# Kernel tuning notes

Hardware: AMD Instinct MI355X
Metric: run time of the kernel (lower is better)

Reference implementation:

```python
import jax, jax.numpy as jnp
import numpy as np

N, L, D = 8, 2048, 128


def setup_inputs() -> dict:
    key = jax.random.key(0)
    k1, k2, k3, k4 = jax.random.split(key, 4)
    x_t = jax.random.normal(k1, (N, L, D), jnp.float32)
    x_f = jax.random.normal(k2, (N, L, D), jnp.float32)
    W = jax.random.normal(k3, (D, D), jnp.float32) / np.sqrt(D)  # proj weight (torch Linear layout)
    b = jax.random.normal(k4, (D,), jnp.float32) * 0.02
    return {"x_t": x_t, "x_f": x_f, "W": W, "b": b}


def _col_score(a, c, scale):
    # softmax attention with zeroed diagonal, then column-sum -> [N, L]
    att = jnp.einsum('nld,nmd->nlm', a, c) * scale
    att = jax.nn.softmax(att, axis=-1)
    att = att * (1.0 - jnp.eye(att.shape[-1], dtype=att.dtype))
    return jnp.sum(att, axis=1)


def _mask(score, time):
    # score: [N, L]; k-th extreme threshold, k = L//2
    k = int(0.5 * score.shape[1])
    if time:
        vals, _ = jax.lax.top_k(score, k)          # k largest, descending
        theta = vals[:, -1:]                        # k-th largest
        return score > theta
    else:
        vals, _ = jax.lax.top_k(-score, k)          # k smallest
        theta = -vals[:, -1:]                       # k-th smallest
        return score <= theta


def reference(x_t, x_f, W, b):
    scale = 1.0 / np.sqrt(W.shape[0])
    pt = x_t @ W.T + b
    pf = x_f @ W.T + b
    score_t = _col_score(pt, pt, scale)
    score_f = _col_score(pf, pf, scale)
    score_tf = _col_score(pt, pf, scale)
    score_ft = _col_score(pf, pt, scale)
    mask_t = _mask(score_t, False)
    mask_f = _mask(score_f, False)
    mask_tf = _mask(score_tf, True)   # computed in original forward (unused in blend)
    mask_ft = _mask(score_ft, True)
    mask_t1 = (mask_t & ~mask_f)[:, :, None]   # [N, L, 1] broadcast over D
    mask_f1 = (mask_f & ~mask_t)[:, :, None]
    x_t1 = jnp.where(mask_t1, x_f, x_t)
    x_f1 = jnp.where(mask_f1, x_t, x_f)
    return (0.5 * (x_t1 + x_t), 0.5 * (x_f1 + x_f))
```

## Files before the change

### kernel.cpp

```cpp
#include <hip/hip_runtime.h>
#include <math.h>

#define LL 2048
#define DD 128
#define NS 16
#define SLAB (LL * DD)
#define SCALE 0.08838834764831845f
#define NT 16
#define NPAIR 136

typedef __attribute__((ext_vector_type(8))) short short8v;
typedef __attribute__((ext_vector_type(4))) float float4v;

__device__ __forceinline__ unsigned int f2bf(float f) {
    unsigned int u = __float_as_uint(f);
    u += 0x7fffu + ((u >> 16) & 1u);
    return u >> 16;
}
__device__ __forceinline__ void pair_decode(int p, int& ib, int& jb) {
    int i = 0;
    while (p >= NT - i) { p -= NT - i; ++i; }
    ib = i; jb = i + p;
}

__device__ __forceinline__ void work_decode(int bx, int by, int& pair, int& ns) {
    const int lin = by * NPAIR + bx;
    const int xcd = lin & 7;
    const int wi  = lin >> 3;
    const int h   = (wi >= NPAIR) ? 1 : 0;
    ns   = xcd + 8 * h;
    pair = wi - NPAIR * h;
}

__device__ __forceinline__ void gl_lds16(const void* g, void* l) {
    __builtin_amdgcn_global_load_lds(
        (const __attribute__((address_space(1))) void*)g,
        (__attribute__((address_space(3))) void*)l, 16, 0, 0);
}

__device__ __forceinline__ void stage_panel(
    const unsigned short* __restrict__ gT, unsigned short* lbuf, int tid)
{
#pragma unroll
    for (int it = 0; it < 2; ++it) {
        const int s   = tid + it * 256;
        const int sb  = (tid & ~63) + it * 256;
        const int row = s >> 2;
        const int oc  = (s & 3) ^ ((row >> 1) & 3);
        gl_lds16(gT + (size_t)row * DD + oc * 8, lbuf + (size_t)sb * 8);
    }
}

__global__ __launch_bounds__(256, 4) void proj_kernel(
    const float* __restrict__ xt, const float* __restrict__ xf,
    const float* __restrict__ W,  const float* __restrict__ bias,
    unsigned short* __restrict__ Ph, unsigned short* __restrict__ Pl)
{
    __shared__ float Alds[64 * 36];
    __shared__ float Blds[128 * 36];
    __shared__ float bs[128];
    const int ns = blockIdx.y;
    const int l0 = blockIdx.x * 64;
    const int src = ns >> 3, n = ns & 7;
    const float* x = (src ? xf : xt) + (size_t)n * LL * DD;
    const int tid = threadIdx.x;
    const int ty = tid >> 4, tx = tid & 15;

    if (tid < 128) bs[tid] = bias[tid];
    __syncthreads();

    float acc[4][8];
#pragma unroll
    for (int i = 0; i < 4; ++i)
#pragma unroll
        for (int j = 0; j < 8; ++j) acc[i][j] = bs[tx + 16 * j];

    for (int kc = 0; kc < 4; ++kc) {
        __syncthreads();
#pragma unroll
        for (int t = 0; t < 2; ++t) {
            int idx = tid + t * 256;
            int r = idx >> 3, k4 = (idx & 7) << 2;
            *(float4*)&Alds[r * 36 + k4] =
                *(const float4*)&x[(size_t)(l0 + r) * DD + kc * 32 + k4];
        }
#pragma unroll
        for (int t = 0; t < 4; ++t) {
            int idx = tid + t * 256;
            int r = idx >> 3, k4 = (idx & 7) << 2;
            *(float4*)&Blds[r * 36 + k4] =
                *(const float4*)&W[(size_t)r * DD + kc * 32 + k4];
        }
        __syncthreads();
#pragma unroll
        for (int k4 = 0; k4 < 32; k4 += 4) {
            float4 a4[4], b4[8];
#pragma unroll
            for (int i = 0; i < 4; ++i) a4[i] = *(const float4*)&Alds[(ty + 16 * i) * 36 + k4];
#pragma unroll
            for (int j = 0; j < 8; ++j) b4[j] = *(const float4*)&Blds[(tx + 16 * j) * 36 + k4];
#pragma unroll
            for (int i = 0; i < 4; ++i)
#pragma unroll
                for (int j = 0; j < 8; ++j) {
                    acc[i][j] = fmaf(a4[i].x, b4[j].x, acc[i][j]);
                    acc[i][j] = fmaf(a4[i].y, b4[j].y, acc[i][j]);
                    acc[i][j] = fmaf(a4[i].z, b4[j].z, acc[i][j]);
                    acc[i][j] = fmaf(a4[i].w, b4[j].w, acc[i][j]);
                }
        }
    }
#pragma unroll
    for (int i = 0; i < 4; ++i) {
        const size_t rowo = (size_t)ns * SLAB + (size_t)(l0 + ty + 16 * i) * DD;
#pragma unroll
        for (int j = 0; j < 8; ++j) {
            float p = acc[i][j];
            unsigned int hb = f2bf(p);
            float hf = __uint_as_float(hb << 16);
            unsigned int lb = f2bf(p - hf);
            Ph[rowo + tx + 16 * j] = (unsigned short)hb;
            Pl[rowo + tx + 16 * j] = (unsigned short)lb;
        }
    }
}

__device__ __forceinline__ void mfma_core(
    const unsigned short* __restrict__ Ph, const unsigned short* __restrict__ Pl,
    int ns, int ib, int jb, int tid,
    unsigned short (*pan)[4096],
    float4v (&acc)[4][4])
{
    const int lane = tid & 63;
    const int quad = lane >> 4, l16 = lane & 15;
    const int wave = tid >> 6;
    const int wr = wave >> 1, wc = wave & 1;
    const bool dg = (ib == jb);

    const unsigned short* sAh = Ph + (size_t)ns * SLAB + (size_t)ib * 128 * DD;
    const unsigned short* sAl = Pl + (size_t)ns * SLAB + (size_t)ib * 128 * DD;
    const unsigned short* sBh = Ph + (size_t)ns * SLAB + (size_t)jb * 128 * DD;
    const unsigned short* sBl = Pl + (size_t)ns * SLAB + (size_t)jb * 128 * DD;

    const unsigned short* alp[4];
#pragma unroll
    for (int rt = 0; rt < 4; ++rt)
        alp[rt] = sAl + (size_t)(wr * 64 + rt * 16 + l16) * DD + quad * 8;

#pragma unroll
    for (int i = 0; i < 4; ++i)
#pragma unroll
        for (int j = 0; j < 4; ++j)
#pragma unroll
            for (int r = 0; r < 4; ++r) acc[i][j][r] = 0.f;

    stage_panel(sAh, pan[0], tid);
    if (!dg) stage_panel(sBh, pan[1], tid);
    stage_panel(sBl, pan[2], tid);
    short8v alr[2][4];
#pragma unroll
    for (int rt = 0; rt < 4; ++rt) alr[0][rt] = *(const short8v*)&alp[rt][0];
    __syncthreads();

#pragma unroll
    for (int kc = 0; kc < 4; ++kc) {
        const int cur = (kc & 1) * 3;
        if (kc < 3) {
            const int nxt = ((kc + 1) & 1) * 3;
            stage_panel(sAh + (kc + 1) * 32, pan[nxt + 0], tid);
            if (!dg) stage_panel(sBh + (kc + 1) * 32, pan[nxt + 1], tid);
            stage_panel(sBl + (kc + 1) * 32, pan[nxt + 2], tid);
#pragma unroll
            for (int rt = 0; rt < 4; ++rt)
                alr[(kc + 1) & 1][rt] = *(const short8v*)&alp[rt][(kc + 1) * 32];
        }
        const unsigned short* AhP = pan[cur + 0];
        const unsigned short* BhP = dg ? pan[cur + 0] : pan[cur + 1];
        const unsigned short* BlP = pan[cur + 2];

        short8v ah[4], bh[4], bl[4];
#pragma unroll
        for (int rt = 0; rt < 4; ++rt) {
            const int r = wr * 64 + rt * 16 + l16;
            const int off = r * 32 + ((quad ^ ((r >> 1) & 3)) << 3);
            ah[rt] = *(const short8v*)&AhP[off];
        }
#pragma unroll
        for (int ct = 0; ct < 4; ++ct) {
            const int r = wc * 64 + ct * 16 + l16;
            const int off = r * 32 + ((quad ^ ((r >> 1) & 3)) << 3);
            bh[ct] = *(const short8v*)&BhP[off];
            bl[ct] = *(const short8v*)&BlP[off];
        }
        __builtin_amdgcn_s_setprio(1);
#pragma unroll
        for (int rt = 0; rt < 4; ++rt)
#pragma unroll
            for (int ct = 0; ct < 4; ++ct) {
                acc[rt][ct] = __builtin_amdgcn_mfma_f32_16x16x32_bf16(ah[rt], bh[ct], acc[rt][ct], 0, 0, 0);
                acc[rt][ct] = __builtin_amdgcn_mfma_f32_16x16x32_bf16(ah[rt], bl[ct], acc[rt][ct], 0, 0, 0);
                acc[rt][ct] = __builtin_amdgcn_mfma_f32_16x16x32_bf16(alr[kc & 1][rt], bh[ct], acc[rt][ct], 0, 0, 0);
            }
        __builtin_amdgcn_s_setprio(0);
        if (kc < 3) __syncthreads();
    }
}

__global__ __launch_bounds__(256, 3) void stats_kernel(
    const unsigned short* __restrict__ Ph, const unsigned short* __restrict__ Pl,
    float* __restrict__ Zpart)
{
    __shared__ unsigned short pan[6][4096];
    __shared__ float Zr[128][2], Zc[128][2];
    int pair, ns;  work_decode(blockIdx.x, blockIdx.y, pair, ns);
    int ib, jb;    pair_decode(pair, ib, jb);
    const int tid = threadIdx.x;
    const int lane = tid & 63, quad = lane >> 4, l16 = lane & 15, wave = tid >> 6;
    const int wr = wave >> 1, wc = wave & 1;

    float4v acc[4][4];
    mfma_core(Ph, Pl, ns, ib, jb, tid, pan, acc);

    float cs[4] = {0.f, 0.f, 0.f, 0.f};
#pragma unroll
    for (int rt = 0; rt < 4; ++rt)
#pragma unroll
        for (int rg = 0; rg < 4; ++rg) {
            float e[4];
            float s = 0.f;
#pragma unroll
            for (int ct = 0; ct < 4; ++ct) {
                e[ct] = __expf(acc[rt][ct][rg] * SCALE);
                s += e[ct]; cs[ct] += e[ct];
            }
            s += __shfl_xor(s, 1);
            s += __shfl_xor(s, 2);
            s += __shfl_xor(s, 4);
            s += __shfl_xor(s, 8);
            if (l16 == 0) Zr[wr * 64 + rt * 16 + quad * 4 + rg][wc] = s;
        }

#pragma unroll
    for (int ct = 0; ct < 4; ++ct) {
        float s = cs[ct];
        s += __shfl_xor(s, 16);
        s += __shfl_xor(s, 32);
        if (quad == 0) Zc[wc * 64 + ct * 16 + l16][wr] = s;
    }
    __syncthreads();
    if (tid < 128) {
        Zpart[(ns * 16 + jb) * LL + ib * 128 + tid] = Zr[tid][0] + Zr[tid][1];
        if (ib != jb)
            Zpart[(ns * 16 + ib) * LL + jb * 128 + tid] = Zc[tid][0] + Zc[tid][1];
    }
}

__global__ __launch_bounds__(256) void reduce_stats_kernel(
    const float* __restrict__ Zpart, float* __restrict__ iZfin)
{
    const int idx = blockIdx.x * 256 + threadIdx.x;
    const int ns = idx >> 11, l = idx & 2047;
    float Z = 0.f;
#pragma unroll
    for (int t = 0; t < 16; ++t) Z += Zpart[(ns * 16 + t) * LL + l];
    iZfin[idx] = 1.0f / Z;
}

__global__ __launch_bounds__(256, 3) void colsum_kernel(
    const unsigned short* __restrict__ Ph, const unsigned short* __restrict__ Pl,
    const float* __restrict__ iZfin, float* __restrict__ Spart)
{
    __shared__ unsigned short pan[6][4096];
    __shared__ float Sr[128][2], Sc[128][2];
    int pair, ns;  work_decode(blockIdx.x, blockIdx.y, pair, ns);
    int ib, jb;    pair_decode(pair, ib, jb);
    const int tid = threadIdx.x;
    const int lane = tid & 63, quad = lane >> 4, l16 = lane & 15, wave = tid >> 6;
    const int wr = wave >> 1, wc = wave & 1;

    float4v acc[4][4];
    mfma_core(Ph, Pl, ns, ib, jb, tid, pan, acc);

    float wrow[4][4];
#pragma unroll
    for (int rt = 0; rt < 4; ++rt)
#pragma unroll
        for (int rg = 0; rg < 4; ++rg)
            wrow[rt][rg] = iZfin[ns * LL + ib * 128 + wr * 64 + rt * 16 + quad * 4 + rg];
    float wcol[4];
#pragma unroll
    for (int ct = 0; ct < 4; ++ct)
        wcol[ct] = iZfin[ns * LL + jb * 128 + wc * 64 + ct * 16 + l16];

    float dsum[4] = {0.f, 0.f, 0.f, 0.f};
#pragma unroll
    for (int rt = 0; rt < 4; ++rt)
#pragma unroll
        for (int rg = 0; rg < 4; ++rg) {
            const int rl = wr * 64 + rt * 16 + quad * 4 + rg;
            float ts = 0.f;
#pragma unroll
            for (int ct = 0; ct < 4; ++ct) {
                float e = __expf(acc[rt][ct][rg] * SCALE);
                bool diag = (ib == jb) && (rl == wc * 64 + ct * 16 + l16);
                dsum[ct] += diag ? 0.f : e * wrow[rt][rg];
                ts += e * wcol[ct];
            }
            if (ib != jb) {
                ts += __shfl_xor(ts, 1);
                ts += __shfl_xor(ts, 2);
                ts += __shfl_xor(ts, 4);
                ts += __shfl_xor(ts, 8);
                if (l16 == 0) Sr[rl][wc] = ts;
            }
        }

#pragma unroll
    for (int ct = 0; ct < 4; ++ct) {
        float s = dsum[ct];
        s += __shfl_xor(s, 16);
        s += __shfl_xor(s, 32);
        if (quad == 0) Sc[wc * 64 + ct * 16 + l16][wr] = s;
    }
    __syncthreads();
    if (tid < 128) {
        Spart[((size_t)ns * LL + jb * 128 + tid) * 16 + ib] = Sc[tid][0] + Sc[tid][1];
        if (ib != jb)
            Spart[((size_t)ns * LL + ib * 128 + tid) * 16 + jb] = Sr[tid][0] + Sr[tid][1];
    }
}

__global__ __launch_bounds__(1024) void mask_kernel(
    const float* __restrict__ Spart, unsigned char* __restrict__ maskbuf)
{
    __shared__ double s[LL];
    const int ns = blockIdx.x;
    const int half = blockIdx.y;
    const int tid = threadIdx.x;
#pragma unroll
    for (int h = 0; h < 2; ++h) {
        int m = tid + h * 1024;
        const float* sp = Spart + ((size_t)ns * LL + m) * 16;
        double a = 0.0;
#pragma unroll
        for (int t = 0; t < 16; ++t) a += (double)sp[t];
        s[m] = a;
    }
    __syncthreads();
    const int i = half * 1024 + tid;
    const double si = s[i];
    int cnt = 0;
    for (int j = 0; j < LL; ++j) cnt += (s[j] < si) ? 1 : 0;
    maskbuf[ns * LL + i] = (cnt < 1024) ? 1 : 0;
}

__global__ __launch_bounds__(256) void blend_kernel(
    const float* __restrict__ xt, const float* __restrict__ xf,
    const unsigned char* __restrict__ maskbuf, float* __restrict__ out)
{
    const int idx4 = blockIdx.x * 256 + threadIdx.x;
    const size_t q = (size_t)idx4 * 4;
    const int row = (int)(q >> 7);
    const float4 a = *(const float4*)(xt + q);
    const float4 b = *(const float4*)(xf + q);
    const int mt = maskbuf[row] & 1;
    const int mf = maskbuf[16384 + row] & 1;
    const bool ct = mt && !mf;
    const bool cf = mf && !mt;
    float4 av;
    av.x = 0.5f * (a.x + b.x);  av.y = 0.5f * (a.y + b.y);
    av.z = 0.5f * (a.z + b.z);  av.w = 0.5f * (a.w + b.w);
    float4 o0 = ct ? av : a;
    float4 o1 = cf ? av : b;
    *(float4*)(out + q)                   = o0;
    *(float4*)(out + (size_t)2097152 + q) = o1;
}

extern "C" void kernel_launch(void* const* d_in, const int* in_sizes, int n_in,
                              void* d_out, int out_size, void* d_ws, size_t ws_size,
                              hipStream_t stream)
{
    const float* xt = (const float*)d_in[0];
    const float* xf = (const float*)d_in[1];
    const float* W  = (const float*)d_in[2];
    const float* b  = (const float*)d_in[3];
    float* out = (float*)d_out;

    unsigned short* Ph = (unsigned short*)d_out;
    unsigned short* Pl = Ph + (size_t)NS * SLAB;

    float* Zpart = (float*)d_ws;
    float* iZfin = Zpart + 16 * 16 * LL;
    float* Spart = iZfin + NS * LL;
    unsigned char* maskbuf = (unsigned char*)(Spart + (size_t)16 * LL * 16);

    proj_kernel<<<dim3(32, NS), 256, 0, stream>>>(xt, xf, W, b, Ph, Pl);
    stats_kernel<<<dim3(NPAIR, NS), 256, 0, stream>>>(Ph, Pl, Zpart);
    reduce_stats_kernel<<<128, 256, 0, stream>>>(Zpart, iZfin);
    colsum_kernel<<<dim3(NPAIR, NS), 256, 0, stream>>>(Ph, Pl, iZfin, Spart);
    mask_kernel<<<dim3(NS, 2), 1024, 0, stream>>>(Spart, maskbuf);
    blend_kernel<<<2048, 256, 0, stream>>>(xt, xf, maskbuf, out);
}
```

Baseline: 230.3 us.

## Triple-buffer LDS panels with vmcnt waits and preload all low-A fragments

Replaces the double-buffered panel staging and full __syncthreads with a three-stage LDS ring that prefetches two k-chunks ahead. It uses explicit s_waitcnt vmcnt counts plus s_barrier so global loads stay in flight across iterations. All four k-chunks of the A low-part fragments are loaded into registers up front. The diagonal-block shortcut that skipped staging B is dropped. LDS per block grows from 6 to 9 panels and launch bounds drop from 3 to 2 blocks per SM, trading occupancy and registers for deeper latency hiding.

New measurement: 249.1 us. +8.1%, slower.

```diff
diff --git a/kernel.cpp b/kernel.cpp
--- a/kernel.cpp
+++ b/kernel.cpp
@@ -135,18 +135,12 @@
     const int quad = lane >> 4, l16 = lane & 15;
     const int wave = tid >> 6;
     const int wr = wave >> 1, wc = wave & 1;
-    const bool dg = (ib == jb);
 
     const unsigned short* sAh = Ph + (size_t)ns * SLAB + (size_t)ib * 128 * DD;
     const unsigned short* sAl = Pl + (size_t)ns * SLAB + (size_t)ib * 128 * DD;
     const unsigned short* sBh = Ph + (size_t)ns * SLAB + (size_t)jb * 128 * DD;
     const unsigned short* sBl = Pl + (size_t)ns * SLAB + (size_t)jb * 128 * DD;
 
-    const unsigned short* alp[4];
-#pragma unroll
-    for (int rt = 0; rt < 4; ++rt)
-        alp[rt] = sAl + (size_t)(wr * 64 + rt * 16 + l16) * DD + quad * 8;
-
 #pragma unroll
     for (int i = 0; i < 4; ++i)
 #pragma unroll
@@ -154,29 +148,36 @@
 #pragma unroll
             for (int r = 0; r < 4; ++r) acc[i][j][r] = 0.f;
 
-    stage_panel(sAh, pan[0], tid);
-    if (!dg) stage_panel(sBh, pan[1], tid);
-    stage_panel(sBl, pan[2], tid);
-    short8v alr[2][4];
-#pragma unroll
-    for (int rt = 0; rt < 4; ++rt) alr[0][rt] = *(const short8v*)&alp[rt][0];
-    __syncthreads();
+    stage_panel(sAh,      pan[0], tid);
+    stage_panel(sBh,      pan[1], tid);
+    stage_panel(sBl,      pan[2], tid);
+    stage_panel(sAh + 32, pan[3], tid);
+    stage_panel(sBh + 32, pan[4], tid);
+    stage_panel(sBl + 32, pan[5], tid);
+    __builtin_amdgcn_sched_barrier(0);
+    asm volatile("s_waitcnt vmcnt(6)" ::: "memory");
+    __builtin_amdgcn_sched_barrier(0);
+
+    short8v alf[4][4];
+#pragma unroll
+    for (int kc = 0; kc < 4; ++kc)
+#pragma unroll
+        for (int rt = 0; rt < 4; ++rt)
+            alf[kc][rt] = *(const short8v*)
+                &sAl[(size_t)(wr * 64 + rt * 16 + l16) * DD + kc * 32 + quad * 8];
+
+    __builtin_amdgcn_s_barrier();
 
 #pragma unroll
     for (int kc = 0; kc < 4; ++kc) {
-        const int cur = (kc & 1) * 3;
-        if (kc < 3) {
-            const int nxt = ((kc + 1) & 1) * 3;
-            stage_panel(sAh + (kc + 1) * 32, pan[nxt + 0], tid);
-            if (!dg) stage_panel(sBh + (kc + 1) * 32, pan[nxt + 1], tid);
-            stage_panel(sBl + (kc + 1) * 32, pan[nxt + 2], tid);
-#pragma unroll
-            for (int rt = 0; rt < 4; ++rt)
-                alr[(kc + 1) & 1][rt] = *(const short8v*)&alp[rt][(kc + 1) * 32];
-        }
-        const unsigned short* AhP = pan[cur + 0];
-        const unsigned short* BhP = dg ? pan[cur + 0] : pan[cur + 1];
-        const unsigned short* BlP = pan[cur + 2];
+        if (kc < 2) {
+            stage_panel(sAh + (kc + 2) * 32, pan[((kc + 2) % 3) * 3 + 0], tid);
+            stage_panel(sBh + (kc + 2) * 32, pan[((kc + 2) % 3) * 3 + 1], tid);
+            stage_panel(sBl + (kc + 2) * 32, pan[((kc + 2) % 3) * 3 + 2], tid);
+        }
+        const unsigned short* AhP = pan[(kc % 3) * 3 + 0];
+        const unsigned short* BhP = pan[(kc % 3) * 3 + 1];
+        const unsigned short* BlP = pan[(kc % 3) * 3 + 2];
 
         short8v ah[4], bh[4], bl[4];
 #pragma unroll
@@ -199,18 +200,21 @@
             for (int ct = 0; ct < 4; ++ct) {
                 acc[rt][ct] = __builtin_amdgcn_mfma_f32_16x16x32_bf16(ah[rt], bh[ct], acc[rt][ct], 0, 0, 0);
                 acc[rt][ct] = __builtin_amdgcn_mfma_f32_16x16x32_bf16(ah[rt], bl[ct], acc[rt][ct], 0, 0, 0);
-                acc[rt][ct] = __builtin_amdgcn_mfma_f32_16x16x32_bf16(alr[kc & 1][rt], bh[ct], acc[rt][ct], 0, 0, 0);
+                acc[rt][ct] = __builtin_amdgcn_mfma_f32_16x16x32_bf16(alf[kc][rt], bh[ct], acc[rt][ct], 0, 0, 0);
             }
         __builtin_amdgcn_s_setprio(0);
-        if (kc < 3) __syncthreads();
-    }
-}
-
-__global__ __launch_bounds__(256, 3) void stats_kernel(
+        __builtin_amdgcn_sched_barrier(0);
+        if (kc < 2)       { asm volatile("s_waitcnt vmcnt(6)" ::: "memory"); }
+        else if (kc == 2) { asm volatile("s_waitcnt vmcnt(0)" ::: "memory"); }
+        if (kc < 3) __builtin_amdgcn_s_barrier();
+    }
+}
+
+__global__ __launch_bounds__(256, 2) void stats_kernel(
     const unsigned short* __restrict__ Ph, const unsigned short* __restrict__ Pl,
     float* __restrict__ Zpart)
 {
-    __shared__ unsigned short pan[6][4096];
+    __shared__ unsigned short pan[9][4096];
     __shared__ float Zr[128][2], Zc[128][2];
     int pair, ns;  work_decode(blockIdx.x, blockIdx.y, pair, ns);
     int ib, jb;    pair_decode(pair, ib, jb);
@@ -266,11 +270,11 @@
     iZfin[idx] = 1.0f / Z;
 }
 
-__global__ __launch_bounds__(256, 3) void colsum_kernel(
+__global__ __launch_bounds__(256, 2) void colsum_kernel(
     const unsigned short* __restrict__ Ph, const unsigned short* __restrict__ Pl,
     const float* __restrict__ iZfin, float* __restrict__ Spart)
 {
-    __shared__ unsigned short pan[6][4096];
+    __shared__ unsigned short pan[9][4096];
     __shared__ float Sr[128][2], Sc[128][2];
     int pair, ns;  work_decode(blockIdx.x, blockIdx.y, pair, ns);
     int ib, jb;    pair_decode(pair, ib, jb);
```
